# Kernel optimization log

Measured on AMD Instinct MI355X. Metric: run time of the kernel, lower is better.

The kernel has to match this reference:

```python
import jax, jax.numpy as jnp
import numpy as np

HID = 128      # hidden_dim
CDIM = 128     # c_dim
NBLK = 5       # n_blocks
RESO = 32      # grid_resolution
G = RESO ** 3  # number of voxels
B, T = 2, 100000


def setup_inputs() -> dict:
    key = jax.random.key(0)
    ks = jax.random.split(key, 8)
    return {
        "points": jax.random.normal(ks[0], (B, T, 3), jnp.float32),
        "index": jax.random.randint(ks[1], (B, 1, T), 0, G, dtype=jnp.int64),
        # fc_pos: Linear(3, 2*HID)
        "fc_pos_w": jax.random.normal(ks[2], (3, 2 * HID), jnp.float32) * 0.1,
        "fc_pos_b": jnp.zeros((2 * HID,), jnp.float32),
        # ResnetBlockFC(2*HID, HID) x NBLK: fc_0 (2H->H), fc_1 (H->H), shortcut (2H->H, no bias)
        "fc0_w": jax.random.normal(ks[3], (NBLK, 2 * HID, HID), jnp.float32) * 0.05,
        "fc0_b": jnp.zeros((NBLK, HID), jnp.float32),
        "fc1_w": jax.random.normal(ks[4], (NBLK, HID, HID), jnp.float32) * 0.05,
        "fc1_b": jnp.zeros((NBLK, HID), jnp.float32),
        "sc_w": jax.random.normal(ks[5], (NBLK, 2 * HID, HID), jnp.float32) * 0.05,
        # fc_c: Linear(HID, CDIM)
        "fc_c_w": jax.random.normal(ks[6], (HID, CDIM), jnp.float32) * 0.05,
        "fc_c_b": jnp.zeros((CDIM,), jnp.float32),
    }


def _resnet_block(x, w0, b0, w1, b1, ws):
    # ResnetBlockFC: net = fc_0(relu(x)); dx = fc_1(relu(net)); out = shortcut(x) + dx
    net = jnp.maximum(x, 0.0) @ w0 + b0
    dx = jnp.maximum(net, 0.0) @ w1 + b1
    return x @ ws + dx


def reference(points, index, fc_pos_w, fc_pos_b, fc0_w, fc0_b, fc1_w, fc1_b, sc_w, fc_c_w, fc_c_b):
    idx = index[:, 0, :]  # [B, T]

    def pool_local(net):
        # scatter_max over voxels, then gather back per point
        seg = jax.vmap(lambda c_b, i_b: jax.ops.segment_max(c_b, i_b, num_segments=G))(net, idx)  # [B,G,H]
        return jnp.take_along_axis(seg, idx[:, :, None], axis=1)  # [B,T,H]; every gathered voxel is non-empty

    net = points @ fc_pos_w + fc_pos_b          # [B,T,2H]
    net = _resnet_block(net, fc0_w[0], fc0_b[0], fc1_w[0], fc1_b[0], sc_w[0])  # [B,T,H]
    for i in range(1, NBLK):
        pooled = pool_local(net)
        net = jnp.concatenate([net, pooled], axis=2)  # [B,T,2H]
        net = _resnet_block(net, fc0_w[i], fc0_b[i], fc1_w[i], fc1_b[i], sc_w[i])

    c = net @ fc_c_w + fc_c_b  # [B,T,CDIM]

    # generate_grid_features: scatter_mean into the 32^3 grid (zeros for empty voxels)
    sums = jax.vmap(lambda c_b, i_b: jax.ops.segment_sum(c_b, i_b, num_segments=G))(c, idx)  # [B,G,CDIM]
    cnts = jax.vmap(lambda i_b: jax.ops.segment_sum(jnp.ones((T,), c.dtype), i_b, num_segments=G))(idx)  # [B,G]
    cnts = cnts[:, :, None]
    mean = jnp.where(cnts > 0, sums / jnp.maximum(cnts, 1.0), 0.0)
    fea_grid = jnp.transpose(mean, (0, 2, 1)).reshape(B, CDIM, RESO, RESO, RESO)
    return fea_grid
```

## Files before the change

### kernel.cpp

```cpp
#include <hip/hip_runtime.h>

#define T_PTS 100000
#define NB 2
#define GCELLS 32768
#define NCELL (NB * GCELLS)
#define HID 128
#define MBLK 64
#define RBPB 1563
#define GRID_RB (NB * RBPB)

typedef __attribute__((ext_vector_type(8))) short bf16x8;
typedef __attribute__((ext_vector_type(4))) float f32x4;

#define MFMA16 __builtin_amdgcn_mfma_f32_16x16x32_bf16

__device__ __forceinline__ unsigned short bf16rne(float f) {
  unsigned u = __float_as_uint(f);
  return (unsigned short)((u + 0x7FFFu + ((u >> 16) & 1u)) >> 16);
}
__device__ __forceinline__ void bf16split(float f, unsigned short& h,
                                          unsigned short& l) {
  h = bf16rne(f);
  l = bf16rne(f - __uint_as_float(((unsigned)h) << 16));
}
__device__ __forceinline__ unsigned packhl(float f) {
  unsigned short h, l;
  bf16split(f, h, l);
  return (((unsigned)h) << 16) | (unsigned)l;
}

union U8 { bf16x8 v; unsigned u[4]; };

__device__ __forceinline__ void up2(unsigned w0, unsigned w1, unsigned& h,
                                    unsigned& l) {
  h = __builtin_amdgcn_perm(w1, w0, 0x07060302u);
  l = __builtin_amdgcn_perm(w1, w0, 0x05040100u);
}

__device__ __forceinline__ void relu2(unsigned qh, unsigned ql, unsigned& rh,
                                      unsigned& rl) {
  const unsigned keep = ((~qh >> 15) & 0x00010001u) * 0xFFFFu;
  rh = qh & keep;
  rl = ql & keep;
}

__device__ __forceinline__ void dma16(const unsigned* g, unsigned* l) {
  __builtin_amdgcn_global_load_lds(
      (const __attribute__((address_space(1))) unsigned*)g,
      (__attribute__((address_space(3))) unsigned*)l, 16, 0, 0);
}

template <int MODE>
__global__ __launch_bounds__(256, 4) void resblock_mfma(
    const void* __restrict__ srcv, const float* __restrict__ posw,
    const float* __restrict__ posb, const unsigned* __restrict__ cell,
    const int* __restrict__ idx, const unsigned short* __restrict__ w0p,
    const float* __restrict__ b0, const unsigned short* __restrict__ w1p,
    const float* __restrict__ b1, const unsigned short* __restrict__ swp,
    unsigned* __restrict__ net_out) {
  __shared__ unsigned lds32[8192];
  const int tid = threadIdx.x;
  const int lane = tid & 63;
  const int wid = tid >> 6;
  const int wc = wid;
  const int b = blockIdx.x / RBPB;
  const int t0 = (blockIdx.x % RBPB) * MBLK;
  const int valid = (T_PTS - t0 < MBLK) ? (T_PTS - t0) : MBLK;

  const int srow = wid * 16 + (lane & 15);
  const int skc4 = (lane >> 4) * 4;
  const int ptc = (t0 + srow < T_PTS) ? srow : (T_PTS - 1 - t0);
  const unsigned* nrowL = nullptr;
  const unsigned* crowL = nullptr;
  float pp0 = 0.f, pp1 = 0.f, pp2 = 0.f;
  if (MODE == 1) {
    const long prow = (long)b * T_PTS + t0 + ptc;
    nrowL = (const unsigned*)srcv + prow * HID;
    crowL = cell + ((long)b * GCELLS + idx[prow]) * HID;
  } else {
    const float* ppp = (const float*)srcv + ((long)b * T_PTS + t0 + ptc) * 3;
    pp0 = ppp[0]; pp1 = ppp[1]; pp2 = ppp[2];
  }

  auto stage_dma = [&](int ks) {
    unsigned* base = &lds32[((ks & 1) << 11) + wid * 256];
    const unsigned* rowp = (ks < 4) ? nrowL : crowL;
    const int ko = ((ks & 3) << 4) + skc4;
    dma16(rowp + ko, base);
    dma16(rowp + 64 + ko, base + 1024);
  };
  auto stage0 = [&](int ks) {
    const int kb = ks * 32 + (lane >> 4) * 8;
    float xv[8];
#pragma unroll
    for (int i = 0; i < 8; i += 4) {
      float4 wa = *(const float4*)(posw + kb + i);
      float4 wb = *(const float4*)(posw + 256 + kb + i);
      float4 wcc = *(const float4*)(posw + 512 + kb + i);
      float4 bb = *(const float4*)(posb + kb + i);
      xv[i + 0] = fmaf(pp0, wa.x, fmaf(pp1, wb.x, fmaf(pp2, wcc.x, bb.x)));
      xv[i + 1] = fmaf(pp0, wa.y, fmaf(pp1, wb.y, fmaf(pp2, wcc.y, bb.y)));
      xv[i + 2] = fmaf(pp0, wa.z, fmaf(pp1, wb.z, fmaf(pp2, wcc.z, bb.z)));
      xv[i + 3] = fmaf(pp0, wa.w, fmaf(pp1, wb.w, fmaf(pp2, wcc.w, bb.w)));
    }
    unsigned ph[8];
#pragma unroll
    for (int i = 0; i < 8; ++i) ph[i] = packhl(xv[i]);
    uint4 xh4, xl4;
    up2(ph[0], ph[1], xh4.x, xl4.x);
    up2(ph[2], ph[3], xh4.y, xl4.y);
    up2(ph[4], ph[5], xh4.z, xl4.z);
    up2(ph[6], ph[7], xh4.w, xl4.w);
    const int db = ((ks & 1) << 11) + wid * 256 + lane * 4;
    *(uint4*)&lds32[db] = xh4;
    *(uint4*)&lds32[db + 1024] = xl4;
  };
  auto load_B = [&](const unsigned short* base, int loOff, int ks, bf16x8* h,
                    bf16x8* l) {
#pragma unroll
    for (int nt = 0; nt < 2; ++nt) {
      const int fi = (ks * 8 + wc * 2 + nt) * 512 + lane * 8;
      h[nt] = *(const bf16x8*)(base + fi);
      l[nt] = *(const bf16x8*)(base + loOff + fi);
    }
  };

  f32x4 accy[4][2], acco[4][2];
#pragma unroll
  for (int i = 0; i < 4; ++i)
#pragma unroll
    for (int j = 0; j < 2; ++j) {
      f32x4 z = {0.f, 0.f, 0.f, 0.f};
      accy[i][j] = z;
      acco[i][j] = z;
    }

  if (MODE == 1) {
    stage_dma(0);
  } else {
    stage0(0);
  }
  __syncthreads();

#pragma unroll 1
  for (int ks = 0; ks < 8; ++ks) {
    const int sb = (ks & 1) << 11;
    bf16x8 b1h[2], b1l[2], b2h[2], b2l[2];
    load_B(w0p, 32768, ks, b1h, b1l);
    load_B(swp, 32768, ks, b2h, b2l);
    if (MODE == 1 && ks < 7) stage_dma(ks + 1);
    __builtin_amdgcn_s_setprio(1);
#pragma unroll
    for (int mt = 0; mt < 4; ++mt) {
      const unsigned* px = &lds32[sb + mt * 256 + lane * 4];
      U8 xh, xl, rh, rl;
      xh.v = *(const bf16x8*)px;
      xl.v = *(const bf16x8*)(px + 1024);
#pragma unroll
      for (int i = 0; i < 4; ++i) relu2(xh.u[i], xl.u[i], rh.u[i], rl.u[i]);
#pragma unroll
      for (int nt = 0; nt < 2; ++nt) {
        accy[mt][nt] = MFMA16(rh.v, b1h[nt], accy[mt][nt], 0, 0, 0);
        accy[mt][nt] = MFMA16(rh.v, b1l[nt], accy[mt][nt], 0, 0, 0);
        accy[mt][nt] = MFMA16(rl.v, b1h[nt], accy[mt][nt], 0, 0, 0);
      }
#pragma unroll
      for (int nt = 0; nt < 2; ++nt) {
        acco[mt][nt] = MFMA16(xh.v, b2h[nt], acco[mt][nt], 0, 0, 0);
        acco[mt][nt] = MFMA16(xh.v, b2l[nt], acco[mt][nt], 0, 0, 0);
        acco[mt][nt] = MFMA16(xl.v, b2h[nt], acco[mt][nt], 0, 0, 0);
      }
    }
    __builtin_amdgcn_s_setprio(0);
    if (MODE == 0 && ks < 7) stage0(ks + 1);
    __syncthreads();
  }

  {
    float b0v[2];
#pragma unroll
    for (int nt = 0; nt < 2; ++nt)
      b0v[nt] = b0[wc * 32 + nt * 16 + (lane & 15)];
#pragma unroll
    for (int mt = 0; mt < 4; ++mt) {
#pragma unroll
      for (int nt = 0; nt < 2; ++nt) {
        const int c = wc * 32 + nt * 16 + (lane & 15);
        const int k2 = c >> 5;
        const int j = c & 7;
        const int lahi = ((c & 31) >> 3) * 16;
#pragma unroll
        for (int r = 0; r < 4; ++r) {
          float h = fmaxf(accy[mt][nt][r] + b0v[nt], 0.f);
          int la = lahi + (lane >> 4) * 4 + r;
          la ^= (la >> 3) & 7;
          lds32[((k2 * 4 + mt) * 64 + la) * 8 + j] = packhl(h);
        }
      }
    }
  }
  __syncthreads();

  {
    const int lar2 = lane ^ ((lane >> 3) & 7);
#pragma unroll
    for (int k2 = 0; k2 < 4; ++k2) {
      bf16x8 ch[2], cl[2];
      load_B(w1p, 16384, k2, ch, cl);
      __builtin_amdgcn_s_setprio(1);
#pragma unroll
      for (int mt = 0; mt < 4; ++mt) {
        const unsigned* p = &lds32[((k2 * 4 + mt) * 64 + lar2) * 8];
        uint4 q1 = *(const uint4*)p;
        uint4 q2 = *(const uint4*)(p + 4);
        unsigned q[8] = {q1.x, q1.y, q1.z, q1.w, q2.x, q2.y, q2.z, q2.w};
        U8 ah, al;
#pragma unroll
        for (int p2 = 0; p2 < 4; ++p2)
          up2(q[2 * p2], q[2 * p2 + 1], ah.u[p2], al.u[p2]);
#pragma unroll
        for (int nt = 0; nt < 2; ++nt) {
          acco[mt][nt] = MFMA16(ah.v, ch[nt], acco[mt][nt], 0, 0, 0);
          acco[mt][nt] = MFMA16(ah.v, cl[nt], acco[mt][nt], 0, 0, 0);
          acco[mt][nt] = MFMA16(al.v, ch[nt], acco[mt][nt], 0, 0, 0);
        }
      }
      __builtin_amdgcn_s_setprio(0);
    }
  }

  {
    float b1v[2];
#pragma unroll
    for (int nt = 0; nt < 2; ++nt)
      b1v[nt] = b1[wc * 32 + nt * 16 + (lane & 15)];
#pragma unroll
    for (int mt = 0; mt < 4; ++mt) {
#pragma unroll
      for (int r = 0; r < 4; ++r) {
        const int row = mt * 16 + (lane >> 4) * 4 + r;
        if (row < valid) {
          unsigned short* op =
              (unsigned short*)(net_out + ((long)b * T_PTS + t0 + row) * HID);
          unsigned short h, l;
          bf16split(acco[mt][0][r] + b1v[0], h, l);
          op[wc * 32 + (lane & 15)] = h;
          op[128 + wc * 32 + (lane & 15)] = l;
          bf16split(acco[mt][1][r] + b1v[1], h, l);
          op[wc * 32 + 16 + (lane & 15)] = h;
          op[128 + wc * 32 + 16 + (lane & 15)] = l;
        }
      }
    }
  }
}

__global__ __launch_bounds__(256, 4) void final_mfma(
    unsigned* __restrict__ net, const unsigned short* __restrict__ wcp,
    const float* __restrict__ bc) {
  __shared__ unsigned lds32[4096];
  const int tid = threadIdx.x;
  const int lane = tid & 63;
  const int wid = tid >> 6;
  const int wc = wid;
  const int b = blockIdx.x / RBPB;
  const int t0 = (blockIdx.x % RBPB) * MBLK;
  const int valid = (T_PTS - t0 < MBLK) ? (T_PTS - t0) : MBLK;

  const int srow = wid * 16 + (lane & 15);
  const int skc4 = (lane >> 4) * 4;
  const int ptc = (t0 + srow < T_PTS) ? srow : (T_PTS - 1 - t0);
  const unsigned* nrowL = net + ((long)b * T_PTS + t0 + ptc) * HID;

  auto stage = [&](int ks) {
    unsigned* base = &lds32[((ks & 1) << 11) + wid * 256];
    const int ko = (ks << 4) + skc4;
    dma16(nrowL + ko, base);
    dma16(nrowL + 64 + ko, base + 1024);
  };
  auto load_B = [&](int ks, bf16x8* h, bf16x8* l) {
#pragma unroll
    for (int nt = 0; nt < 2; ++nt) {
      const int fi = (ks * 8 + wc * 2 + nt) * 512 + lane * 8;
      h[nt] = *(const bf16x8*)(wcp + fi);
      l[nt] = *(const bf16x8*)(wcp + 16384 + fi);
    }
  };

  f32x4 acc[4][2];
#pragma unroll
  for (int i = 0; i < 4; ++i)
#pragma unroll
    for (int j = 0; j < 2; ++j) {
      f32x4 z = {0.f, 0.f, 0.f, 0.f};
      acc[i][j] = z;
    }

  stage(0);
  __syncthreads();

#pragma unroll 1
  for (int ks = 0; ks < 4; ++ks) {
    const int sb = (ks & 1) << 11;
    bf16x8 ch[2], cl[2];
    load_B(ks, ch, cl);
    if (ks < 3) stage(ks + 1);
    __builtin_amdgcn_s_setprio(1);
#pragma unroll
    for (int mt = 0; mt < 4; ++mt) {
      const unsigned* px = &lds32[sb + mt * 256 + lane * 4];
      bf16x8 xh = *(const bf16x8*)px;
      bf16x8 xl = *(const bf16x8*)(px + 1024);
#pragma unroll
      for (int nt = 0; nt < 2; ++nt) {
        acc[mt][nt] = MFMA16(xh, ch[nt], acc[mt][nt], 0, 0, 0);
        acc[mt][nt] = MFMA16(xh, cl[nt], acc[mt][nt], 0, 0, 0);
        acc[mt][nt] = MFMA16(xl, ch[nt], acc[mt][nt], 0, 0, 0);
      }
    }
    __builtin_amdgcn_s_setprio(0);
    __syncthreads();
  }

  float* fout = (float*)net;
  float bcv[2];
#pragma unroll
  for (int nt = 0; nt < 2; ++nt)
    bcv[nt] = bc[wc * 32 + nt * 16 + (lane & 15)];
#pragma unroll
  for (int mt = 0; mt < 4; ++mt) {
#pragma unroll
    for (int r = 0; r < 4; ++r) {
      const int row = mt * 16 + (lane >> 4) * 4 + r;
      if (row < valid) {
        float* op = fout + ((long)b * T_PTS + t0 + row) * HID;
        op[wc * 32 + (lane & 15)] = acc[mt][0][r] + bcv[0];
        op[wc * 32 + 16 + (lane & 15)] = acc[mt][1][r] + bcv[1];
      }
    }
  }
}

__global__ void pack_weights(const float* __restrict__ fc0,
                             const float* __restrict__ fc1,
                             const float* __restrict__ sc,
                             const float* __restrict__ fcc,
                             unsigned short* __restrict__ w0p,
                             unsigned short* __restrict__ w1p,
                             unsigned short* __restrict__ swp,
                             unsigned short* __restrict__ wcp) {
  int gid = blockIdx.x * 256 + threadIdx.x;
  const float* src;
  unsigned short* dst;
  int K, e;
  if (gid < 163840) { src = fc0; dst = w0p; K = 256; e = gid; }
  else if (gid < 327680) { src = sc; dst = swp; K = 256; e = gid - 163840; }
  else if (gid < 409600) { src = fc1; dst = w1p; K = 128; e = gid - 327680; }
  else if (gid < 425984) { src = fcc; dst = wcp; K = 128; e = gid - 409600; }
  else return;
  const int mat = e / (K * 128);
  const int r = e - mat * K * 128;
  const int k = r >> 7, n = r & 127;
  const float x = src[e];
  unsigned short hi, lo;
  bf16split(x, hi, lo);
  const int ks = k >> 5, lg = (k >> 3) & 3, j = k & 7;
  const int l = lg * 16 + (n & 15), nt = n >> 4;
  unsigned short* mb = dst + (long)mat * K * 256;
  const int off = ((ks * 8 + nt) * 64 + l) * 8 + j;
  mb[off] = hi;
  mb[off + K * 128] = lo;
}

__global__ void zero_i32(int* __restrict__ p, int n) {
  const int i = blockIdx.x * 256 + threadIdx.x;
  if (i < n) p[i] = 0;
}

__global__ void count_csr(const int* __restrict__ idx, int* __restrict__ curs) {
  const int gid = blockIdx.x * 256 + threadIdx.x;
  if (gid >= NB * T_PTS) return;
  const int b = gid / T_PTS;
  atomicAdd(&curs[b * GCELLS + idx[gid]], 1);
}

__global__ __launch_bounds__(1024) void scan_csr(const int* __restrict__ cnt,
                                                 int* __restrict__ offsets) {
  __shared__ int part[1024];
  const int t = threadIdx.x;
  const int base = t * (NCELL / 1024);
  int s = 0;
  for (int i = 0; i < NCELL / 1024; ++i) s += cnt[base + i];
  part[t] = s;
  __syncthreads();
  for (int d = 1; d < 1024; d <<= 1) {
    int v = (t >= d) ? part[t - d] : 0;
    __syncthreads();
    part[t] += v;
    __syncthreads();
  }
  int run = (t == 0) ? 0 : part[t - 1];
  for (int i = 0; i < NCELL / 1024; ++i) {
    offsets[base + i] = run;
    run += cnt[base + i];
  }
  if (t == 1023) offsets[NCELL] = run;
}

__global__ void scatter_csr(const int* __restrict__ idx,
                            const int* __restrict__ offsets,
                            int* __restrict__ curs, int* __restrict__ perm) {
  const int gid = blockIdx.x * 256 + threadIdx.x;
  if (gid >= NB * T_PTS) return;
  const int b = gid / T_PTS;
  const int cellk = b * GCELLS + idx[gid];
  const int slot = offsets[cellk] + atomicAdd(&curs[cellk], 1);
  perm[slot] = gid;
}

__global__ __launch_bounds__(256) void pool_csr(const unsigned* __restrict__ net,
                                                const int* __restrict__ perm,
                                                const int* __restrict__ offsets,
                                                unsigned* __restrict__ cellf) {
  const int cellk = blockIdx.x * 4 + (threadIdx.x >> 6);
  const int lane = threadIdx.x & 63;
  const int s0 = offsets[cellk], s1 = offsets[cellk + 1];
  if (s0 >= s1) return;
  float m0 = -3.402823466e38f, m1 = -3.402823466e38f;
  unsigned h0 = 0u, l0 = 0u, h1 = 0u, l1 = 0u;
  for (int j = s0; j < s1; ++j) {
    const long row = perm[j];
    const unsigned* rp = net + row * HID;
    unsigned hi = rp[lane];
    unsigned lo = rp[64 + lane];
    float v0 = __uint_as_float(hi << 16) + __uint_as_float(lo << 16);
    float v1 = __uint_as_float(hi & 0xFFFF0000u) +
               __uint_as_float(lo & 0xFFFF0000u);
    if (v0 > m0) { m0 = v0; h0 = hi; l0 = lo; }
    if (v1 > m1) { m1 = v1; h1 = hi; l1 = lo; }
  }
  unsigned* cp = cellf + (long)cellk * HID;
  cp[lane] = (h0 & 0xFFFFu) | (h1 & 0xFFFF0000u);
  cp[64 + lane] = (l0 & 0xFFFFu) | (l1 & 0xFFFF0000u);
}

__global__ __launch_bounds__(256) void cellsum_csr(
    const float* __restrict__ c, const int* __restrict__ perm,
    const int* __restrict__ offsets, float* __restrict__ sums) {
  const int cellk = blockIdx.x * 4 + (threadIdx.x >> 6);
  const int lane = threadIdx.x & 63;
  const int s0 = offsets[cellk], s1 = offsets[cellk + 1];
  if (s0 >= s1) return;
  float2 m = {0.f, 0.f};
  for (int j = s0; j < s1; ++j) {
    const long row = perm[j];
    float2 v = *(const float2*)(c + row * HID + lane * 2);
    m.x += v.x;
    m.y += v.y;
  }
  *(float2*)(sums + (long)cellk * HID + lane * 2) = m;
}

__global__ void mean_kernel(const float* __restrict__ sums,
                            const int* __restrict__ offsets,
                            float* __restrict__ out) {
  const long gid = (long)blockIdx.x * 256 + threadIdx.x;
  if (gid >= (long)NB * HID * GCELLS) return;
  const int g = (int)(gid % GCELLS);
  const int c = (int)((gid / GCELLS) % HID);
  const int b = (int)(gid / ((long)HID * GCELLS));
  const int cellk = b * GCELLS + g;
  const int cnt = offsets[cellk + 1] - offsets[cellk];
  out[gid] = cnt > 0 ? sums[(long)cellk * HID + c] / (float)cnt : 0.f;
}

extern "C" void kernel_launch(void* const* d_in, const int* in_sizes, int n_in,
                              void* d_out, int out_size, void* d_ws,
                              size_t ws_size, hipStream_t stream) {
  const float* points = (const float*)d_in[0];
  const int* idx = (const int*)d_in[1];
  const float* fc_pos_w = (const float*)d_in[2];
  const float* fc_pos_b = (const float*)d_in[3];
  const float* fc0_w = (const float*)d_in[4];
  const float* fc0_b = (const float*)d_in[5];
  const float* fc1_w = (const float*)d_in[6];
  const float* fc1_b = (const float*)d_in[7];
  const float* sc_w = (const float*)d_in[8];
  const float* fc_c_w = (const float*)d_in[9];
  const float* fc_c_b = (const float*)d_in[10];
  float* out = (float*)d_out;

  const long NET_BYTES = (long)NB * T_PTS * HID * 4;
  const long CELL_BYTES = (long)NB * GCELLS * HID * 4;
  unsigned* net = (unsigned*)d_ws;
  unsigned* cellf = (unsigned*)((char*)d_ws + NET_BYTES);
  float* sums = (float*)cellf;
  int* offsets = (int*)((char*)d_ws + NET_BYTES + CELL_BYTES);

  unsigned short* packs = (unsigned short*)d_out;
  unsigned short* w0p = packs;
  unsigned short* swp = packs + 327680;
  unsigned short* w1p = packs + 655360;
  unsigned short* wcp = packs + 819200;
  int* curs = (int*)((char*)d_out + (2l << 20));
  int* perm = (int*)((char*)d_out + (3l << 20));

  const int GRID_PTS = (NB * T_PTS + 255) / 256;
  const int GRID_ZERO = (NCELL + 255) / 256;
  const int GRID_CELL = NCELL / 4;
  const int GRID_MEAN = NB * HID * GCELLS / 256;

  pack_weights<<<1664, 256, 0, stream>>>(fc0_w, fc1_w, sc_w, fc_c_w, w0p, w1p,
                                         swp, wcp);

  zero_i32<<<GRID_ZERO, 256, 0, stream>>>(curs, NCELL);
  count_csr<<<GRID_PTS, 256, 0, stream>>>(idx, curs);
  scan_csr<<<1, 1024, 0, stream>>>(curs, offsets);
  zero_i32<<<GRID_ZERO, 256, 0, stream>>>(curs, NCELL);
  scatter_csr<<<GRID_PTS, 256, 0, stream>>>(idx, offsets, curs, perm);

  resblock_mfma<0><<<GRID_RB, 256, 0, stream>>>(
      points, fc_pos_w, fc_pos_b, nullptr, nullptr, w0p, fc0_b, w1p, fc1_b,
      swp, net);

  for (int i = 1; i < 5; ++i) {
    pool_csr<<<GRID_CELL, 256, 0, stream>>>(net, perm, offsets, cellf);
    resblock_mfma<1><<<GRID_RB, 256, 0, stream>>>(
        net, nullptr, nullptr, cellf, idx, w0p + (long)i * 65536,
        fc0_b + i * HID, w1p + (long)i * 32768, fc1_b + i * HID,
        swp + (long)i * 65536, net);
  }

  final_mfma<<<GRID_RB, 256, 0, stream>>>(net, wcp, fc_c_b);
  cellsum_csr<<<GRID_CELL, 256, 0, stream>>>((const float*)net, perm, offsets,
                                             sums);
  mean_kernel<<<GRID_MEAN, 256, 0, stream>>>(sums, offsets, out);
}
```

Before: 799.6 us.

## Store per-point activations in cell-sorted order to make pooling reads contiguous

The first resblock now gathers input points through the CSR permutation, so every later activation buffer is laid out in cell-sorted row order. The pooling and cell-sum kernels then read consecutive rows instead of indirecting through perm, and the resblock reads its pooled cell feature through a per-row cell index array. The batch split and tail masks go away because 200000 rows divide evenly into 64-row tiles. The final output is a per-cell mean, so row order does not affect it; the cost is an extra vcell array and a scattered read of points.

```diff
diff --git a/kernel.cpp b/kernel.cpp
--- a/kernel.cpp
+++ b/kernel.cpp
@@ -2,12 +2,12 @@
 
 #define T_PTS 100000
 #define NB 2
+#define NROWS (NB * T_PTS)
 #define GCELLS 32768
 #define NCELL (NB * GCELLS)
 #define HID 128
 #define MBLK 64
-#define RBPB 1563
-#define GRID_RB (NB * RBPB)
+#define GRID_RB (NROWS / MBLK)
 
 typedef __attribute__((ext_vector_type(8))) short bf16x8;
 typedef __attribute__((ext_vector_type(4))) float f32x4;
@@ -54,31 +54,28 @@
 __global__ __launch_bounds__(256, 4) void resblock_mfma(
     const void* __restrict__ srcv, const float* __restrict__ posw,
     const float* __restrict__ posb, const unsigned* __restrict__ cell,
-    const int* __restrict__ idx, const unsigned short* __restrict__ w0p,
-    const float* __restrict__ b0, const unsigned short* __restrict__ w1p,
-    const float* __restrict__ b1, const unsigned short* __restrict__ swp,
-    unsigned* __restrict__ net_out) {
+    const int* __restrict__ perm, const int* __restrict__ vcell,
+    const unsigned short* __restrict__ w0p, const float* __restrict__ b0,
+    const unsigned short* __restrict__ w1p, const float* __restrict__ b1,
+    const unsigned short* __restrict__ swp, unsigned* __restrict__ net_out) {
   __shared__ unsigned lds32[8192];
   const int tid = threadIdx.x;
   const int lane = tid & 63;
   const int wid = tid >> 6;
   const int wc = wid;
-  const int b = blockIdx.x / RBPB;
-  const int t0 = (blockIdx.x % RBPB) * MBLK;
-  const int valid = (T_PTS - t0 < MBLK) ? (T_PTS - t0) : MBLK;
+  const int t0 = blockIdx.x * MBLK;
 
   const int srow = wid * 16 + (lane & 15);
   const int skc4 = (lane >> 4) * 4;
-  const int ptc = (t0 + srow < T_PTS) ? srow : (T_PTS - 1 - t0);
+  const long vrow = (long)t0 + srow;
   const unsigned* nrowL = nullptr;
   const unsigned* crowL = nullptr;
   float pp0 = 0.f, pp1 = 0.f, pp2 = 0.f;
   if (MODE == 1) {
-    const long prow = (long)b * T_PTS + t0 + ptc;
-    nrowL = (const unsigned*)srcv + prow * HID;
-    crowL = cell + ((long)b * GCELLS + idx[prow]) * HID;
+    nrowL = (const unsigned*)srcv + vrow * HID;
+    crowL = cell + (long)vcell[vrow] * HID;
   } else {
-    const float* ppp = (const float*)srcv + ((long)b * T_PTS + t0 + ptc) * 3;
+    const float* ppp = (const float*)srcv + (long)perm[vrow] * 3;
     pp0 = ppp[0]; pp1 = ppp[1]; pp2 = ppp[2];
   }
 
@@ -239,17 +236,15 @@
 #pragma unroll
       for (int r = 0; r < 4; ++r) {
         const int row = mt * 16 + (lane >> 4) * 4 + r;
-        if (row < valid) {
-          unsigned short* op =
-              (unsigned short*)(net_out + ((long)b * T_PTS + t0 + row) * HID);
-          unsigned short h, l;
-          bf16split(acco[mt][0][r] + b1v[0], h, l);
-          op[wc * 32 + (lane & 15)] = h;
-          op[128 + wc * 32 + (lane & 15)] = l;
-          bf16split(acco[mt][1][r] + b1v[1], h, l);
-          op[wc * 32 + 16 + (lane & 15)] = h;
-          op[128 + wc * 32 + 16 + (lane & 15)] = l;
-        }
+        unsigned short* op =
+            (unsigned short*)(net_out + ((long)t0 + row) * HID);
+        unsigned short h, l;
+        bf16split(acco[mt][0][r] + b1v[0], h, l);
+        op[wc * 32 + (lane & 15)] = h;
+        op[128 + wc * 32 + (lane & 15)] = l;
+        bf16split(acco[mt][1][r] + b1v[1], h, l);
+        op[wc * 32 + 16 + (lane & 15)] = h;
+        op[128 + wc * 32 + 16 + (lane & 15)] = l;
       }
     }
   }
@@ -263,14 +258,11 @@
   const int lane = tid & 63;
   const int wid = tid >> 6;
   const int wc = wid;
-  const int b = blockIdx.x / RBPB;
-  const int t0 = (blockIdx.x % RBPB) * MBLK;
-  const int valid = (T_PTS - t0 < MBLK) ? (T_PTS - t0) : MBLK;
+  const int t0 = blockIdx.x * MBLK;
 
   const int srow = wid * 16 + (lane & 15);
   const int skc4 = (lane >> 4) * 4;
-  const int ptc = (t0 + srow < T_PTS) ? srow : (T_PTS - 1 - t0);
-  const unsigned* nrowL = net + ((long)b * T_PTS + t0 + ptc) * HID;
+  const unsigned* nrowL = net + ((long)t0 + srow) * HID;
 
   auto stage = [&](int ks) {
     unsigned* base = &lds32[((ks & 1) << 11) + wid * 256];
@@ -332,11 +324,9 @@
 #pragma unroll
     for (int r = 0; r < 4; ++r) {
       const int row = mt * 16 + (lane >> 4) * 4 + r;
-      if (row < valid) {
-        float* op = fout + ((long)b * T_PTS + t0 + row) * HID;
-        op[wc * 32 + (lane & 15)] = acc[mt][0][r] + bcv[0];
-        op[wc * 32 + 16 + (lane & 15)] = acc[mt][1][r] + bcv[1];
-      }
+      float* op = fout + ((long)t0 + row) * HID;
+      op[wc * 32 + (lane & 15)] = acc[mt][0][r] + bcv[0];
+      op[wc * 32 + 16 + (lane & 15)] = acc[mt][1][r] + bcv[1];
     }
   }
 }
@@ -379,7 +369,7 @@
 
 __global__ void count_csr(const int* __restrict__ idx, int* __restrict__ curs) {
   const int gid = blockIdx.x * 256 + threadIdx.x;
-  if (gid >= NB * T_PTS) return;
+  if (gid >= NROWS) return;
   const int b = gid / T_PTS;
   atomicAdd(&curs[b * GCELLS + idx[gid]], 1);
 }
@@ -409,17 +399,18 @@
 
 __global__ void scatter_csr(const int* __restrict__ idx,
                             const int* __restrict__ offsets,
-                            int* __restrict__ curs, int* __restrict__ perm) {
+                            int* __restrict__ curs, int* __restrict__ perm,
+                            int* __restrict__ vcell) {
   const int gid = blockIdx.x * 256 + threadIdx.x;
-  if (gid >= NB * T_PTS) return;
+  if (gid >= NROWS) return;
   const int b = gid / T_PTS;
   const int cellk = b * GCELLS + idx[gid];
   const int slot = offsets[cellk] + atomicAdd(&curs[cellk], 1);
   perm[slot] = gid;
+  vcell[slot] = cellk;
 }
 
 __global__ __launch_bounds__(256) void pool_csr(const unsigned* __restrict__ net,
-                                                const int* __restrict__ perm,
                                                 const int* __restrict__ offsets,
                                                 unsigned* __restrict__ cellf) {
   const int cellk = blockIdx.x * 4 + (threadIdx.x >> 6);
@@ -428,9 +419,8 @@
   if (s0 >= s1) return;
   float m0 = -3.402823466e38f, m1 = -3.402823466e38f;
   unsigned h0 = 0u, l0 = 0u, h1 = 0u, l1 = 0u;
-  for (int j = s0; j < s1; ++j) {
-    const long row = perm[j];
-    const unsigned* rp = net + row * HID;
+  for (int row = s0; row < s1; ++row) {
+    const unsigned* rp = net + (long)row * HID;
     unsigned hi = rp[lane];
     unsigned lo = rp[64 + lane];
     float v0 = __uint_as_float(hi << 16) + __uint_as_float(lo << 16);
@@ -445,16 +435,15 @@
 }
 
 __global__ __launch_bounds__(256) void cellsum_csr(
-    const float* __restrict__ c, const int* __restrict__ perm,
-    const int* __restrict__ offsets, float* __restrict__ sums) {
+    const float* __restrict__ c, const int* __restrict__ offsets,
+    float* __restrict__ sums) {
   const int cellk = blockIdx.x * 4 + (threadIdx.x >> 6);
   const int lane = threadIdx.x & 63;
   const int s0 = offsets[cellk], s1 = offsets[cellk + 1];
   if (s0 >= s1) return;
   float2 m = {0.f, 0.f};
-  for (int j = s0; j < s1; ++j) {
-    const long row = perm[j];
-    float2 v = *(const float2*)(c + row * HID + lane * 2);
+  for (int row = s0; row < s1; ++row) {
+    float2 v = *(const float2*)(c + (long)row * HID + lane * 2);
     m.x += v.x;
     m.y += v.y;
   }
@@ -490,8 +479,8 @@
   const float* fc_c_b = (const float*)d_in[10];
   float* out = (float*)d_out;
 
-  const long NET_BYTES = (long)NB * T_PTS * HID * 4;
-  const long CELL_BYTES = (long)NB * GCELLS * HID * 4;
+  const long NET_BYTES = (long)NROWS * HID * 4;
+  const long CELL_BYTES = (long)NCELL * HID * 4;
   unsigned* net = (unsigned*)d_ws;
   unsigned* cellf = (unsigned*)((char*)d_ws + NET_BYTES);
   float* sums = (float*)cellf;
@@ -504,8 +493,9 @@
   unsigned short* wcp = packs + 819200;
   int* curs = (int*)((char*)d_out + (2l << 20));
   int* perm = (int*)((char*)d_out + (3l << 20));
-
-  const int GRID_PTS = (NB * T_PTS + 255) / 256;
+  int* vcell = (int*)((char*)d_out + (4l << 20));
+
+  const int GRID_PTS = (NROWS + 255) / 256;
   const int GRID_ZERO = (NCELL + 255) / 256;
   const int GRID_CELL = NCELL / 4;
   const int GRID_MEAN = NB * HID * GCELLS / 256;
@@ -517,22 +507,21 @@
   count_csr<<<GRID_PTS, 256, 0, stream>>>(idx, curs);
   scan_csr<<<1, 1024, 0, stream>>>(curs, offsets);
   zero_i32<<<GRID_ZERO, 256, 0, stream>>>(curs, NCELL);
-  scatter_csr<<<GRID_PTS, 256, 0, stream>>>(idx, offsets, curs, perm);
+  scatter_csr<<<GRID_PTS, 256, 0, stream>>>(idx, offsets, curs, perm, vcell);
 
   resblock_mfma<0><<<GRID_RB, 256, 0, stream>>>(
-      points, fc_pos_w, fc_pos_b, nullptr, nullptr, w0p, fc0_b, w1p, fc1_b,
-      swp, net);
+      points, fc_pos_w, fc_pos_b, nullptr, perm, vcell, w0p, fc0_b, w1p,
+      fc1_b, swp, net);
 
   for (int i = 1; i < 5; ++i) {
-    pool_csr<<<GRID_CELL, 256, 0, stream>>>(net, perm, offsets, cellf);
+    pool_csr<<<GRID_CELL, 256, 0, stream>>>(net, offsets, cellf);
     resblock_mfma<1><<<GRID_RB, 256, 0, stream>>>(
-        net, nullptr, nullptr, cellf, idx, w0p + (long)i * 65536,
+        net, nullptr, nullptr, cellf, perm, vcell, w0p + (long)i * 65536,
         fc0_b + i * HID, w1p + (long)i * 32768, fc1_b + i * HID,
         swp + (long)i * 65536, net);
   }
 
   final_mfma<<<GRID_RB, 256, 0, stream>>>(net, wcp, fc_c_b);
-  cellsum_csr<<<GRID_CELL, 256, 0, stream>>>((const float*)net, perm, offsets,
-                                             sums);
+  cellsum_csr<<<GRID_CELL, 256, 0, stream>>>((const float*)net, offsets, sums);
   mean_kernel<<<GRID_MEAN, 256, 0, stream>>>(sums, offsets, out);
 }
```

Result: faster. 755.3 us (-5.5%).
